# Optimization experiments

Measured on AMD Instinct MI355X. Metric: run time of the kernel, lower is better.

The kernel has to match this reference:

```python
import jax, jax.numpy as jnp
import numpy as np

EPS = 1e-18

_SOBEL_H = jnp.array([[-1., -2., -1.], [0., 0., 0.], [1., 2., 1.]], dtype=jnp.float32)


def _sobel_mag(x, eps):
    # x: [B,1,H,W]; depth-1 3x3 conv with 'same' padding, two fixed kernels
    wh = _SOBEL_H.reshape(1, 1, 3, 3).astype(x.dtype)   # horizontal kernel
    wv = _SOBEL_H.T.reshape(1, 1, 3, 3).astype(x.dtype)  # vertical kernel
    dn = jax.lax.conv_dimension_numbers(x.shape, wh.shape, ('NCHW', 'OIHW', 'NCHW'))
    gv = jax.lax.conv_general_dilated(x, wv, (1, 1), 'SAME', dimension_numbers=dn)
    gh = jax.lax.conv_general_dilated(x, wh, (1, 1), 'SAME', dimension_numbers=dn)
    return jnp.sqrt(gv * gv + gh * gh + eps)


def setup_inputs() -> dict:
    key = jax.random.key(0)
    k1, k2 = jax.random.split(key)
    shape = (64, 1, 512, 512)
    y_p = jax.random.uniform(k1, shape, dtype=jnp.float32)
    y_t = jax.random.uniform(k2, shape, dtype=jnp.float32)
    return {"y_p": y_p, "y_t": y_t}


def reference(y_p, y_t):
    eps = EPS
    ypg = _sobel_mag(y_p, eps)
    ytg = _sobel_mag(y_t, eps)
    out = (ytg - ypg) ** 2
    mask = (out == 0.0).astype(out.dtype)
    out = out + mask * eps
    out = jnp.sqrt(out + eps) * (1.0 - mask)
    return jnp.mean(out)
```

## Files before the change

kernel.cpp:

```cpp
#include <hip/hip_runtime.h>

#define IMG_W 512
#define IMG_H 512
#define BATCH 64
#define SLAB_ROWS 16
#define SLABS (IMG_H / SLAB_ROWS)
#define NBLOCKS (BATCH * SLABS)
#define NPIX (BATCH * IMG_W * IMG_H)

typedef float f32x4 __attribute__((ext_vector_type(4)));

__device__ __forceinline__ float fast_sqrtf(float x) {
    return __builtin_amdgcn_sqrtf(x);
}


#define GLOAD(dst, ptr)                                                        \
    asm volatile("global_load_dwordx4 %0, %1, off" : "=v"(dst) : "v"(ptr))

#define LOADR(I, A, B, IMG)                                                    \
    {                                                                          \
        int yy = ty - 1 + (I);                                                 \
        int yc = yy < 0 ? 0 : (yy > IMG_H - 1 ? IMG_H - 1 : yy);               \
        const float* r_ = (IMG) + ((size_t)yc << 9) + x0;                      \
        GLOAD(A, r_);                                                          \
        GLOAD(B, r_ + 4);                                                      \
    }

#define MKWIN(W, A, B)                                                         \
    float W[10];                                                               \
    {                                                                          \
        float l_ = __shfl_up((B)[3], 1, 64);                                   \
        float r_ = __shfl_down((A)[0], 1, 64);                                 \
        W[0] = (lane == 0) ? 0.f : l_;                                         \
        W[1] = (A)[0]; W[2] = (A)[1]; W[3] = (A)[2]; W[4] = (A)[3];            \
        W[5] = (B)[0]; W[6] = (B)[1]; W[7] = (B)[2]; W[8] = (B)[3];            \
        W[9] = (lane == 63) ? 0.f : r_;                                        \
    }

#define MKHS(HS, W)                                                            \
    float HS[8];                                                               \
    _Pragma("unroll")                                                          \
    for (int j = 0; j < 8; ++j)                                                \
        HS[j] = fmaf(2.f, W[j + 1], W[j]) + W[j + 2];

#define DO_OUT_P(O, WA, WB, WC, HSA, HSC)                                      \
    {                                                                          \
        float c_[10];                                                          \
        _Pragma("unroll")                                                      \
        for (int k = 0; k < 10; ++k)                                           \
            c_[k] = fmaf(2.f, WB[k], WA[k]) + WC[k];                           \
        _Pragma("unroll")                                                      \
        for (int j = 0; j < 8; ++j) {                                          \
            float gh = HSC[j] - HSA[j];                                        \
            float gv = c_[j + 2] - c_[j];                                      \
            magp[O][j] = fast_sqrtf(fmaf(gv, gv, fmaf(gh, gh, 1e-18f)));       \
        }                                                                      \
    }

#define DO_OUT_T(O, WA, WB, WC, HSA, HSC)                                      \
    {                                                                          \
        float c_[10];                                                          \
        _Pragma("unroll")                                                      \
        for (int k = 0; k < 10; ++k)                                           \
            c_[k] = fmaf(2.f, WB[k], WA[k]) + WC[k];                           \
        _Pragma("unroll")                                                      \
        for (int j = 0; j < 8; ++j) {                                          \
            float gh = HSC[j] - HSA[j];                                        \
            float gv = c_[j + 2] - c_[j];                                      \
            float mt = fast_sqrtf(fmaf(gv, gv, fmaf(gh, gh, 1e-18f)));         \
            lsum += fabsf(mt - magp[O][j]);     \
        }                                                                      \
    }

#define SOBEL_P(A0, B0, A1, B1, A2, B2, A3, B3, A4, B4, A5, B5)                \
    {                                                                          \
        MKWIN(w0_, A0, B0) MKWIN(w1_, A1, B1) MKWIN(w2_, A2, B2)               \
        MKWIN(w3_, A3, B3) MKWIN(w4_, A4, B4) MKWIN(w5_, A5, B5)               \
        MKHS(h0_, w0_) MKHS(h1_, w1_) MKHS(h2_, w2_)                           \
        MKHS(h3_, w3_) MKHS(h4_, w4_) MKHS(h5_, w5_)                           \
        DO_OUT_P(0, w0_, w1_, w2_, h0_, h2_)                                   \
        DO_OUT_P(1, w1_, w2_, w3_, h1_, h3_)                                   \
        DO_OUT_P(2, w2_, w3_, w4_, h2_, h4_)                                   \
        DO_OUT_P(3, w3_, w4_, w5_, h3_, h5_)                                   \
    }

#define SOBEL_T(A0, B0, A1, B1, A2, B2, A3, B3, A4, B4, A5, B5)                \
    {                                                                          \
        MKWIN(w0_, A0, B0) MKWIN(w1_, A1, B1) MKWIN(w2_, A2, B2)               \
        MKWIN(w3_, A3, B3) MKWIN(w4_, A4, B4) MKWIN(w5_, A5, B5)               \
        MKHS(h0_, w0_) MKHS(h1_, w1_) MKHS(h2_, w2_)                           \
        MKHS(h3_, w3_) MKHS(h4_, w4_) MKHS(h5_, w5_)                           \
        DO_OUT_T(0, w0_, w1_, w2_, h0_, h2_)                                   \
        DO_OUT_T(1, w1_, w2_, w3_, h1_, h3_)                                   \
        DO_OUT_T(2, w2_, w3_, w4_, h2_, h4_)                                   \
        DO_OUT_T(3, w3_, w4_, w5_, h3_, h5_)                                   \
    }

__global__ __launch_bounds__(256) void sobel_loss_kernel(
    const float* __restrict__ yp, const float* __restrict__ yt,
    float* __restrict__ bsums)
{
    __shared__ float wred[4];

    const int tid  = threadIdx.x;
    const int lane = tid & 63;
    const int bid  = blockIdx.x;
    const int b    = bid >> 5;
    const int slab = bid & (SLABS - 1);
    const int ty   = slab * SLAB_ROWS + ((tid >> 6) << 2);
    const int x0   = lane << 3;

    const float* imgp = yp + ((size_t)b << 18);
    const float* imgt = yt + ((size_t)b << 18);

    f32x4 A0p, B0p, A1p, B1p, A2p, B2p, A3p, B3p, A4p, B4p, A5p, B5p;
    f32x4 A0t, B0t, A1t, B1t, A2t, B2t, A3t, B3t, A4t, B4t, A5t, B5t;

    LOADR(0, A0p, B0p, imgp) LOADR(1, A1p, B1p, imgp) LOADR(2, A2p, B2p, imgp)
    LOADR(3, A3p, B3p, imgp) LOADR(4, A4p, B4p, imgp) LOADR(5, A5p, B5p, imgp)
    LOADR(0, A0t, B0t, imgt) LOADR(1, A1t, B1t, imgt) LOADR(2, A2t, B2t, imgt)
    LOADR(3, A3t, B3t, imgt) LOADR(4, A4t, B4t, imgt) LOADR(5, A5t, B5t, imgt)

    asm volatile("s_waitcnt vmcnt(12)"
                 : "+v"(A0p), "+v"(B0p), "+v"(A1p), "+v"(B1p),
                   "+v"(A2p), "+v"(B2p), "+v"(A3p), "+v"(B3p),
                   "+v"(A4p), "+v"(B4p), "+v"(A5p), "+v"(B5p));

    const f32x4 z4 = {0.f, 0.f, 0.f, 0.f};
    if (ty == 0)         { A0p = z4; B0p = z4; }
    if (ty + 4 == IMG_H) { A5p = z4; B5p = z4; }

    float magp[4][8];
    float lsum = 0.f;
    SOBEL_P(A0p, B0p, A1p, B1p, A2p, B2p, A3p, B3p, A4p, B4p, A5p, B5p)

    asm volatile("s_waitcnt vmcnt(0)"
                 : "+v"(A0t), "+v"(B0t), "+v"(A1t), "+v"(B1t),
                   "+v"(A2t), "+v"(B2t), "+v"(A3t), "+v"(B3t),
                   "+v"(A4t), "+v"(B4t), "+v"(A5t), "+v"(B5t));

    if (ty == 0)         { A0t = z4; B0t = z4; }
    if (ty + 4 == IMG_H) { A5t = z4; B5t = z4; }

    SOBEL_T(A0t, B0t, A1t, B1t, A2t, B2t, A3t, B3t, A4t, B4t, A5t, B5t)

#pragma unroll
    for (int off = 32; off > 0; off >>= 1)
        lsum += __shfl_down(lsum, off, 64);
    if (lane == 0) wred[tid >> 6] = lsum;
    __syncthreads();
    if (tid == 0)
        bsums[bid] = wred[0] + wred[1] + wred[2] + wred[3];
}

__global__ __launch_bounds__(256) void reduce_final(
    const float* __restrict__ bsums, float* __restrict__ out)
{
    __shared__ float wred[4];
    const int tid = threadIdx.x;
    float s = 0.f;
    for (int i = tid; i < NBLOCKS; i += 256) s += bsums[i];
#pragma unroll
    for (int off = 32; off > 0; off >>= 1)
        s += __shfl_down(s, off, 64);
    if ((tid & 63) == 0) wred[tid >> 6] = s;
    __syncthreads();
    if (tid == 0)
        out[0] = (wred[0] + wred[1] + wred[2] + wred[3]) * (1.0f / (float)NPIX);
}

extern "C" void kernel_launch(void* const* d_in, const int* in_sizes, int n_in,
                              void* d_out, int out_size, void* d_ws, size_t ws_size,
                              hipStream_t stream) {
    const float* yp = (const float*)d_in[0];
    const float* yt = (const float*)d_in[1];
    float* out = (float*)d_out;

    float* bsums = (float*)d_ws;
    sobel_loss_kernel<<<NBLOCKS, 256, 0, stream>>>(yp, yt, bsums);
    reduce_final<<<1, 256, 0, stream>>>(bsums, out);
}
```

Baseline: 144.4 us.

## Stage slab rows into LDS via global_load_lds and remap block order

Replaces the per-wave direct global loads of 6 overlapping rows with a cooperative stage of 18 rows per image into LDS using global_load_lds. Each wave then reads its rows from LDS, which removes the duplicated halo row fetches across waves. Blocks are also remapped with a stride-8 swizzle, likely to spread work across XCDs. In exchange the p and t loads are now serialized behind barriers, so the t load no longer overlaps the p compute, and the kernel uses about 36KB of LDS, which may cut occupancy.

After: 147.3 us. 2.0% more time.

```diff
diff --git a/kernel.cpp b/kernel.cpp
--- a/kernel.cpp
+++ b/kernel.cpp
@@ -7,6 +7,7 @@
 #define SLABS (IMG_H / SLAB_ROWS)
 #define NBLOCKS (BATCH * SLABS)
 #define NPIX (BATCH * IMG_W * IMG_H)
+#define LDS_ROWS 18
 
 typedef float f32x4 __attribute__((ext_vector_type(4)));
 
@@ -15,17 +16,12 @@
 }
 
 
-#define GLOAD(dst, ptr)                                                        \
-    asm volatile("global_load_dwordx4 %0, %1, off" : "=v"(dst) : "v"(ptr))
-
-#define LOADR(I, A, B, IMG)                                                    \
-    {                                                                          \
-        int yy = ty - 1 + (I);                                                 \
-        int yc = yy < 0 ? 0 : (yy > IMG_H - 1 ? IMG_H - 1 : yy);               \
-        const float* r_ = (IMG) + ((size_t)yc << 9) + x0;                      \
-        GLOAD(A, r_);                                                          \
-        GLOAD(B, r_ + 4);                                                      \
-    }
+typedef const __attribute__((address_space(1))) void gas_void;
+typedef __attribute__((address_space(3))) void las_void;
+
+__device__ __forceinline__ void gload_lds16(const float* g, float* l) {
+    __builtin_amdgcn_global_load_lds((gas_void*)g, (las_void*)l, 16, 0, 0);
+}
 
 #define MKWIN(W, A, B)                                                         \
     float W[10];                                                               \
@@ -97,61 +93,83 @@
         DO_OUT_T(3, w3_, w4_, w5_, h3_, h5_)                                   \
     }
 
+#define STAGE_IMG(IMG)                                                         \
+    {                                                                          \
+        _Pragma("unroll")                                                      \
+        for (int k = 0; k < 9; ++k) {                                          \
+            const int c = w * 9 + k;            \
+            int ys = row0 + (c >> 1);                                          \
+            ys = ys < 0 ? 0 : (ys > IMG_H - 1 ? IMG_H - 1 : ys);               \
+            gload_lds16((IMG) + ((size_t)ys << 9) + ((c & 1) << 8) + (lane << 2), \
+                        smem + (c << 8) + (lane << 2));                        \
+        }                                                                      \
+    }
+
+#define LDS_ROWS_TO_REGS()                                                     \
+    A0 = s4[rbase + 0 * 128 + cidx]; B0 = s4[rbase + 0 * 128 + cidx + 1];      \
+    A1 = s4[rbase + 1 * 128 + cidx]; B1 = s4[rbase + 1 * 128 + cidx + 1];      \
+    A2 = s4[rbase + 2 * 128 + cidx]; B2 = s4[rbase + 2 * 128 + cidx + 1];      \
+    A3 = s4[rbase + 3 * 128 + cidx]; B3 = s4[rbase + 3 * 128 + cidx + 1];      \
+    A4 = s4[rbase + 4 * 128 + cidx]; B4 = s4[rbase + 4 * 128 + cidx + 1];      \
+    A5 = s4[rbase + 5 * 128 + cidx]; B5 = s4[rbase + 5 * 128 + cidx + 1];
+
 __global__ __launch_bounds__(256) void sobel_loss_kernel(
     const float* __restrict__ yp, const float* __restrict__ yt,
     float* __restrict__ bsums)
 {
+    __shared__ float smem[LDS_ROWS * IMG_W];
     __shared__ float wred[4];
 
     const int tid  = threadIdx.x;
     const int lane = tid & 63;
-    const int bid  = blockIdx.x;
+    const int w    = tid >> 6;
+
+    const int bid0 = blockIdx.x;
+    const int bid  = (bid0 & 7) * (NBLOCKS / 8) + (bid0 >> 3);
+
     const int b    = bid >> 5;
     const int slab = bid & (SLABS - 1);
-    const int ty   = slab * SLAB_ROWS + ((tid >> 6) << 2);
-    const int x0   = lane << 3;
+    const int row0 = slab * SLAB_ROWS - 1;
+    const int ty   = slab * SLAB_ROWS + (w << 2);
 
     const float* imgp = yp + ((size_t)b << 18);
     const float* imgt = yt + ((size_t)b << 18);
 
-    f32x4 A0p, B0p, A1p, B1p, A2p, B2p, A3p, B3p, A4p, B4p, A5p, B5p;
-    f32x4 A0t, B0t, A1t, B1t, A2t, B2t, A3t, B3t, A4t, B4t, A5t, B5t;
-
-    LOADR(0, A0p, B0p, imgp) LOADR(1, A1p, B1p, imgp) LOADR(2, A2p, B2p, imgp)
-    LOADR(3, A3p, B3p, imgp) LOADR(4, A4p, B4p, imgp) LOADR(5, A5p, B5p, imgp)
-    LOADR(0, A0t, B0t, imgt) LOADR(1, A1t, B1t, imgt) LOADR(2, A2t, B2t, imgt)
-    LOADR(3, A3t, B3t, imgt) LOADR(4, A4t, B4t, imgt) LOADR(5, A5t, B5t, imgt)
-
-    asm volatile("s_waitcnt vmcnt(12)"
-                 : "+v"(A0p), "+v"(B0p), "+v"(A1p), "+v"(B1p),
-                   "+v"(A2p), "+v"(B2p), "+v"(A3p), "+v"(B3p),
-                   "+v"(A4p), "+v"(B4p), "+v"(A5p), "+v"(B5p));
+    const f32x4* s4 = (const f32x4*)smem;
+    const int rbase = (w << 2) * (IMG_W / 4);
+    const int cidx  = lane << 1;
 
     const f32x4 z4 = {0.f, 0.f, 0.f, 0.f};
-    if (ty == 0)         { A0p = z4; B0p = z4; }
-    if (ty + 4 == IMG_H) { A5p = z4; B5p = z4; }
+    f32x4 A0, B0, A1, B1, A2, B2, A3, B3, A4, B4, A5, B5;
 
     float magp[4][8];
     float lsum = 0.f;
-    SOBEL_P(A0p, B0p, A1p, B1p, A2p, B2p, A3p, B3p, A4p, B4p, A5p, B5p)
-
-    asm volatile("s_waitcnt vmcnt(0)"
-                 : "+v"(A0t), "+v"(B0t), "+v"(A1t), "+v"(B1t),
-                   "+v"(A2t), "+v"(B2t), "+v"(A3t), "+v"(B3t),
-                   "+v"(A4t), "+v"(B4t), "+v"(A5t), "+v"(B5t));
-
-    if (ty == 0)         { A0t = z4; B0t = z4; }
-    if (ty + 4 == IMG_H) { A5t = z4; B5t = z4; }
-
-    SOBEL_T(A0t, B0t, A1t, B1t, A2t, B2t, A3t, B3t, A4t, B4t, A5t, B5t)
+
+    STAGE_IMG(imgp)
+    __syncthreads();
+
+    LDS_ROWS_TO_REGS()
+    if (ty == 0)         { A0 = z4; B0 = z4; }
+    if (ty + 4 == IMG_H) { A5 = z4; B5 = z4; }
+    SOBEL_P(A0, B0, A1, B1, A2, B2, A3, B3, A4, B4, A5, B5)
+
+    __syncthreads();
+
+    STAGE_IMG(imgt)
+    __syncthreads();
+
+    LDS_ROWS_TO_REGS()
+    if (ty == 0)         { A0 = z4; B0 = z4; }
+    if (ty + 4 == IMG_H) { A5 = z4; B5 = z4; }
+    SOBEL_T(A0, B0, A1, B1, A2, B2, A3, B3, A4, B4, A5, B5)
 
 #pragma unroll
     for (int off = 32; off > 0; off >>= 1)
         lsum += __shfl_down(lsum, off, 64);
-    if (lane == 0) wred[tid >> 6] = lsum;
+    if (lane == 0) wred[w] = lsum;
     __syncthreads();
     if (tid == 0)
-        bsums[bid] = wred[0] + wred[1] + wred[2] + wred[3];
+        bsums[blockIdx.x] = wred[0] + wred[1] + wred[2] + wred[3];
 }
 
 __global__ __launch_bounds__(256) void reduce_final(
```

## Stage y_p slab into LDS via direct global-to-LDS loads, remap block order

Applied to the files above, without the earlier changes.

The predicted-image slab (18 rows including halo) is now loaded directly into shared memory with global_load_lds, so rows overlapping between the four wavefronts are fetched once instead of re-read from global memory. Each wave then reads its six rows from LDS into registers after a barrier. The target image keeps the old per-wave register loads. Block IDs are also permuted in a stride-8 pattern, likely to spread neighbouring slabs across XCDs/caches. This adds 36KB LDS per block, which may lower occupancy, and adds a barrier.

After: 148.3 us. 1.03x slower.

```diff
diff --git a/kernel.cpp b/kernel.cpp
--- a/kernel.cpp
+++ b/kernel.cpp
@@ -7,6 +7,7 @@
 #define SLABS (IMG_H / SLAB_ROWS)
 #define NBLOCKS (BATCH * SLABS)
 #define NPIX (BATCH * IMG_W * IMG_H)
+#define LDS_ROWS 18
 
 typedef float f32x4 __attribute__((ext_vector_type(4)));
 
@@ -14,6 +15,13 @@
     return __builtin_amdgcn_sqrtf(x);
 }
 
+
+typedef const __attribute__((address_space(1))) void gas_void;
+typedef __attribute__((address_space(3))) void las_void;
+
+__device__ __forceinline__ void gload_lds16(const float* g, float* l) {
+    __builtin_amdgcn_global_load_lds((gas_void*)g, (las_void*)l, 16, 0, 0);
+}
 
 #define GLOAD(dst, ptr)                                                        \
     asm volatile("global_load_dwordx4 %0, %1, off" : "=v"(dst) : "v"(ptr))
@@ -97,61 +105,88 @@
         DO_OUT_T(3, w3_, w4_, w5_, h3_, h5_)                                   \
     }
 
+#define STAGE_IMG(IMG)                                                         \
+    {                                                                          \
+        _Pragma("unroll")                                                      \
+        for (int k = 0; k < 9; ++k) {                                          \
+            const int c = w * 9 + k;            \
+            int ys = row0 + (c >> 1);                                          \
+            ys = ys < 0 ? 0 : (ys > IMG_H - 1 ? IMG_H - 1 : ys);               \
+            gload_lds16((IMG) + ((size_t)ys << 9) + ((c & 1) << 8) + (lane << 2), \
+                        smem + (c << 8) + (lane << 2));                        \
+        }                                                                      \
+    }
+
+#define LDS_ROWS_TO_REGS()                                                     \
+    A0p = s4[rbase + 0 * 128 + cidx]; B0p = s4[rbase + 0 * 128 + cidx + 1];    \
+    A1p = s4[rbase + 1 * 128 + cidx]; B1p = s4[rbase + 1 * 128 + cidx + 1];    \
+    A2p = s4[rbase + 2 * 128 + cidx]; B2p = s4[rbase + 2 * 128 + cidx + 1];    \
+    A3p = s4[rbase + 3 * 128 + cidx]; B3p = s4[rbase + 3 * 128 + cidx + 1];    \
+    A4p = s4[rbase + 4 * 128 + cidx]; B4p = s4[rbase + 4 * 128 + cidx + 1];    \
+    A5p = s4[rbase + 5 * 128 + cidx]; B5p = s4[rbase + 5 * 128 + cidx + 1];
+
 __global__ __launch_bounds__(256) void sobel_loss_kernel(
     const float* __restrict__ yp, const float* __restrict__ yt,
     float* __restrict__ bsums)
 {
+    __shared__ float smem[LDS_ROWS * IMG_W];
     __shared__ float wred[4];
 
     const int tid  = threadIdx.x;
     const int lane = tid & 63;
-    const int bid  = blockIdx.x;
+    const int w    = tid >> 6;
+
+    const int bid0 = blockIdx.x;
+    const int bid  = (bid0 & 7) * (NBLOCKS / 8) + (bid0 >> 3);
+
     const int b    = bid >> 5;
     const int slab = bid & (SLABS - 1);
-    const int ty   = slab * SLAB_ROWS + ((tid >> 6) << 2);
+    const int row0 = slab * SLAB_ROWS - 1;
+    const int ty   = slab * SLAB_ROWS + (w << 2);
     const int x0   = lane << 3;
 
     const float* imgp = yp + ((size_t)b << 18);
     const float* imgt = yt + ((size_t)b << 18);
 
+    const f32x4* s4 = (const f32x4*)smem;
+    const int rbase = (w << 2) * (IMG_W / 4);
+    const int cidx  = lane << 1;
+
+    const f32x4 z4 = {0.f, 0.f, 0.f, 0.f};
     f32x4 A0p, B0p, A1p, B1p, A2p, B2p, A3p, B3p, A4p, B4p, A5p, B5p;
     f32x4 A0t, B0t, A1t, B1t, A2t, B2t, A3t, B3t, A4t, B4t, A5t, B5t;
 
-    LOADR(0, A0p, B0p, imgp) LOADR(1, A1p, B1p, imgp) LOADR(2, A2p, B2p, imgp)
-    LOADR(3, A3p, B3p, imgp) LOADR(4, A4p, B4p, imgp) LOADR(5, A5p, B5p, imgp)
+    float magp[4][8];
+    float lsum = 0.f;
+
+    STAGE_IMG(imgp)
     LOADR(0, A0t, B0t, imgt) LOADR(1, A1t, B1t, imgt) LOADR(2, A2t, B2t, imgt)
     LOADR(3, A3t, B3t, imgt) LOADR(4, A4t, B4t, imgt) LOADR(5, A5t, B5t, imgt)
 
-    asm volatile("s_waitcnt vmcnt(12)"
-                 : "+v"(A0p), "+v"(B0p), "+v"(A1p), "+v"(B1p),
-                   "+v"(A2p), "+v"(B2p), "+v"(A3p), "+v"(B3p),
-                   "+v"(A4p), "+v"(B4p), "+v"(A5p), "+v"(B5p));
-
-    const f32x4 z4 = {0.f, 0.f, 0.f, 0.f};
+    asm volatile("s_waitcnt vmcnt(12)" ::: "memory");
+    __builtin_amdgcn_s_barrier();
+    __builtin_amdgcn_sched_barrier(0);
+
+    LDS_ROWS_TO_REGS()
     if (ty == 0)         { A0p = z4; B0p = z4; }
     if (ty + 4 == IMG_H) { A5p = z4; B5p = z4; }
-
-    float magp[4][8];
-    float lsum = 0.f;
     SOBEL_P(A0p, B0p, A1p, B1p, A2p, B2p, A3p, B3p, A4p, B4p, A5p, B5p)
 
     asm volatile("s_waitcnt vmcnt(0)"
                  : "+v"(A0t), "+v"(B0t), "+v"(A1t), "+v"(B1t),
                    "+v"(A2t), "+v"(B2t), "+v"(A3t), "+v"(B3t),
                    "+v"(A4t), "+v"(B4t), "+v"(A5t), "+v"(B5t));
-
     if (ty == 0)         { A0t = z4; B0t = z4; }
     if (ty + 4 == IMG_H) { A5t = z4; B5t = z4; }
-
     SOBEL_T(A0t, B0t, A1t, B1t, A2t, B2t, A3t, B3t, A4t, B4t, A5t, B5t)
 
 #pragma unroll
     for (int off = 32; off > 0; off >>= 1)
         lsum += __shfl_down(lsum, off, 64);
-    if (lane == 0) wred[tid >> 6] = lsum;
+    if (lane == 0) wred[w] = lsum;
     __syncthreads();
     if (tid == 0)
-        bsums[bid] = wred[0] + wred[1] + wred[2] + wred[3];
+        bsums[blockIdx.x] = wred[0] + wred[1] + wred[2] + wred[3];
 }
 
 __global__ __launch_bounds__(256) void reduce_final(
```

## Stream 16-row strips per wave with rolling row buffers and prefetch pipeline

Applied to the files above, without the earlier changes.

Each wave now processes a 16-row strip instead of a 4-row slab. It keeps a 6-deep ring of loaded rows and 3-deep horizontal-sum rings, issues loads three rows ahead, and overlaps them with compute through explicit vmcnt waits. This cuts halo re-reads from 6 loaded rows per 4 outputs to 18 per 16, and shrinks the grid to a quarter of the blocks. The risks are higher register pressure from the 2-wave launch bound and fewer blocks available to hide latency.

Result: no change. 144.9 us (+0.4%).

```diff
diff --git a/kernel.cpp b/kernel.cpp
--- a/kernel.cpp
+++ b/kernel.cpp
@@ -3,9 +3,10 @@
 #define IMG_W 512
 #define IMG_H 512
 #define BATCH 64
-#define SLAB_ROWS 16
-#define SLABS (IMG_H / SLAB_ROWS)
-#define NBLOCKS (BATCH * SLABS)
+#define STRIP_ROWS 16
+#define STRIPS_PER_IMG (IMG_H / STRIP_ROWS)
+#define NSTRIPS (BATCH * STRIPS_PER_IMG)
+#define NB_MAIN (NSTRIPS / 4)
 #define NPIX (BATCH * IMG_W * IMG_H)
 
 typedef float f32x4 __attribute__((ext_vector_type(4)));
@@ -18,86 +19,97 @@
 #define GLOAD(dst, ptr)                                                        \
     asm volatile("global_load_dwordx4 %0, %1, off" : "=v"(dst) : "v"(ptr))
 
-#define LOADR(I, A, B, IMG)                                                    \
+#define S6(k) (((k) + 1) % 6)
+#define S3(k) (((k) + 1) % 3)
+
+#define WEL(A, B, HL, HR, k, j)                                                \
+    ((j) == 0 ? HL[S3(k)]                                                      \
+              : ((j) == 9 ? HR[S3(k)]                                          \
+                          : ((j) <= 4 ? A[S6(k)][(j) - 1] : B[S6(k)][(j) - 5])))
+
+#define ISSUE(k, A, B, IMG)                                                    \
     {                                                                          \
-        int yy = ty - 1 + (I);                                                 \
-        int yc = yy < 0 ? 0 : (yy > IMG_H - 1 ? IMG_H - 1 : yy);               \
-        const float* r_ = (IMG) + ((size_t)yc << 9) + x0;                      \
-        GLOAD(A, r_);                                                          \
-        GLOAD(B, r_ + 4);                                                      \
+        int gy_ = stripy + (k);                                                \
+        gy_ = gy_ < 0 ? 0 : (gy_ > IMG_H - 1 ? IMG_H - 1 : gy_);               \
+        const float* r_ = (IMG) + ((size_t)gy_ << 9) + x0;                     \
+        GLOAD(A[S6(k)], r_);                                                   \
+        GLOAD(B[S6(k)], r_ + 4);                                               \
     }
 
-#define MKWIN(W, A, B)                                                         \
-    float W[10];                                                               \
+#define PREP(k, A, B, HL, HR, HS)                                              \
     {                                                                          \
-        float l_ = __shfl_up((B)[3], 1, 64);                                   \
-        float r_ = __shfl_down((A)[0], 1, 64);                                 \
-        W[0] = (lane == 0) ? 0.f : l_;                                         \
-        W[1] = (A)[0]; W[2] = (A)[1]; W[3] = (A)[2]; W[4] = (A)[3];            \
-        W[5] = (B)[0]; W[6] = (B)[1]; W[7] = (B)[2]; W[8] = (B)[3];            \
-        W[9] = (lane == 63) ? 0.f : r_;                                        \
+        float l_ = __shfl_up(B[S6(k)][3], 1, 64);                              \
+        float r_ = __shfl_down(A[S6(k)][0], 1, 64);                            \
+        HL[S3(k)] = (lane == 0) ? 0.f : l_;                                    \
+        HR[S3(k)] = (lane == 63) ? 0.f : r_;                                   \
+        _Pragma("unroll")                                                      \
+        for (int j = 0; j < 8; ++j)                                            \
+            HS[S3(k)][j] = fmaf(2.f, WEL(A, B, HL, HR, k, j + 1),              \
+                                WEL(A, B, HL, HR, k, j)) +                     \
+                           WEL(A, B, HL, HR, k, j + 2);                        \
     }
 
-#define MKHS(HS, W)                                                            \
-    float HS[8];                                                               \
-    _Pragma("unroll")                                                          \
-    for (int j = 0; j < 8; ++j)                                                \
-        HS[j] = fmaf(2.f, W[j + 1], W[j]) + W[j + 2];
-
-#define DO_OUT_P(O, WA, WB, WC, HSA, HSC)                                      \
+#define OUT_P(r)                                                               \
     {                                                                          \
-        float c_[10];                                                          \
+        float c9_[10];                                                         \
         _Pragma("unroll")                                                      \
-        for (int k = 0; k < 10; ++k)                                           \
-            c_[k] = fmaf(2.f, WB[k], WA[k]) + WC[k];                           \
+        for (int j = 0; j < 10; ++j)                                           \
+            c9_[j] = fmaf(2.f, WEL(pA, pB, hlP, hrP, (r), j),                  \
+                          WEL(pA, pB, hlP, hrP, (r)-1, j)) +                   \
+                     WEL(pA, pB, hlP, hrP, (r) + 1, j);                        \
         _Pragma("unroll")                                                      \
         for (int j = 0; j < 8; ++j) {                                          \
-            float gh = HSC[j] - HSA[j];                                        \
-            float gv = c_[j + 2] - c_[j];                                      \
-            magp[O][j] = fast_sqrtf(fmaf(gv, gv, fmaf(gh, gh, 1e-18f)));       \
+            float gh = hsP[S3((r) + 1)][j] - hsP[S3((r)-1)][j];                \
+            float gv = c9_[j + 2] - c9_[j];                                    \
+            magrow[j] = fast_sqrtf(fmaf(gv, gv, fmaf(gh, gh, 1e-18f)));        \
         }                                                                      \
     }
 
-#define DO_OUT_T(O, WA, WB, WC, HSA, HSC)                                      \
+#define OUT_T(r)                                                               \
     {                                                                          \
-        float c_[10];                                                          \
+        float c9_[10];                                                         \
         _Pragma("unroll")                                                      \
-        for (int k = 0; k < 10; ++k)                                           \
-            c_[k] = fmaf(2.f, WB[k], WA[k]) + WC[k];                           \
+        for (int j = 0; j < 10; ++j)                                           \
+            c9_[j] = fmaf(2.f, WEL(tA, tB, hlT, hrT, (r), j),                  \
+                          WEL(tA, tB, hlT, hrT, (r)-1, j)) +                   \
+                     WEL(tA, tB, hlT, hrT, (r) + 1, j);                        \
         _Pragma("unroll")                                                      \
         for (int j = 0; j < 8; ++j) {                                          \
-            float gh = HSC[j] - HSA[j];                                        \
-            float gv = c_[j + 2] - c_[j];                                      \
+            float gh = hsT[S3((r) + 1)][j] - hsT[S3((r)-1)][j];                \
+            float gv = c9_[j + 2] - c9_[j];                                    \
             float mt = fast_sqrtf(fmaf(gv, gv, fmaf(gh, gh, 1e-18f)));         \
-            lsum += fabsf(mt - magp[O][j]);     \
+            lsum += fabsf(mt - magrow[j]);      \
         }                                                                      \
     }
 
-#define SOBEL_P(A0, B0, A1, B1, A2, B2, A3, B3, A4, B4, A5, B5)                \
+#define ITER(r, WP, WT)                                                        \
     {                                                                          \
-        MKWIN(w0_, A0, B0) MKWIN(w1_, A1, B1) MKWIN(w2_, A2, B2)               \
-        MKWIN(w3_, A3, B3) MKWIN(w4_, A4, B4) MKWIN(w5_, A5, B5)               \
-        MKHS(h0_, w0_) MKHS(h1_, w1_) MKHS(h2_, w2_)                           \
-        MKHS(h3_, w3_) MKHS(h4_, w4_) MKHS(h5_, w5_)                           \
-        DO_OUT_P(0, w0_, w1_, w2_, h0_, h2_)                                   \
-        DO_OUT_P(1, w1_, w2_, w3_, h1_, h3_)                                   \
-        DO_OUT_P(2, w2_, w3_, w4_, h2_, h4_)                                   \
-        DO_OUT_P(3, w3_, w4_, w5_, h3_, h5_)                                   \
+        float magrow[8];                                                       \
+        asm volatile("s_waitcnt vmcnt(" #WP ")" ::: "memory");                 \
+        __builtin_amdgcn_sched_barrier(0);                                     \
+        if ((r) == 0 && stop_) { pA[S6(-1)] = z4; pB[S6(-1)] = z4; }           \
+        if ((r) == 15 && sbot_) { pA[S6(16)] = z4; pB[S6(16)] = z4; }          \
+        if ((r) == 0) {                                                        \
+            PREP(-1, pA, pB, hlP, hrP, hsP)                                    \
+            PREP(0, pA, pB, hlP, hrP, hsP)                                     \
+        }                                                                      \
+        PREP((r) + 1, pA, pB, hlP, hrP, hsP)                                   \
+        if ((r) <= 13) ISSUE((r) + 3, pA, pB, imgp)                            \
+        OUT_P(r)                                                               \
+        asm volatile("s_waitcnt vmcnt(" #WT ")" ::: "memory");                 \
+        __builtin_amdgcn_sched_barrier(0);                                     \
+        if ((r) == 0 && stop_) { tA[S6(-1)] = z4; tB[S6(-1)] = z4; }           \
+        if ((r) == 15 && sbot_) { tA[S6(16)] = z4; tB[S6(16)] = z4; }          \
+        if ((r) == 0) {                                                        \
+            PREP(-1, tA, tB, hlT, hrT, hsT)                                    \
+            PREP(0, tA, tB, hlT, hrT, hsT)                                     \
+        }                                                                      \
+        PREP((r) + 1, tA, tB, hlT, hrT, hsT)                                   \
+        if ((r) <= 13) ISSUE((r) + 3, tA, tB, imgt)                            \
+        OUT_T(r)                                                               \
     }
 
-#define SOBEL_T(A0, B0, A1, B1, A2, B2, A3, B3, A4, B4, A5, B5)                \
-    {                                                                          \
-        MKWIN(w0_, A0, B0) MKWIN(w1_, A1, B1) MKWIN(w2_, A2, B2)               \
-        MKWIN(w3_, A3, B3) MKWIN(w4_, A4, B4) MKWIN(w5_, A5, B5)               \
-        MKHS(h0_, w0_) MKHS(h1_, w1_) MKHS(h2_, w2_)                           \
-        MKHS(h3_, w3_) MKHS(h4_, w4_) MKHS(h5_, w5_)                           \
-        DO_OUT_T(0, w0_, w1_, w2_, h0_, h2_)                                   \
-        DO_OUT_T(1, w1_, w2_, w3_, h1_, h3_)                                   \
-        DO_OUT_T(2, w2_, w3_, w4_, h2_, h4_)                                   \
-        DO_OUT_T(3, w3_, w4_, w5_, h3_, h5_)                                   \
-    }
-
-__global__ __launch_bounds__(256) void sobel_loss_kernel(
+__global__ __launch_bounds__(256, 2) void sobel_loss_kernel(
     const float* __restrict__ yp, const float* __restrict__ yt,
     float* __restrict__ bsums)
 {
@@ -105,50 +117,41 @@
 
     const int tid  = threadIdx.x;
     const int lane = tid & 63;
-    const int bid  = blockIdx.x;
-    const int b    = bid >> 5;
-    const int slab = bid & (SLABS - 1);
-    const int ty   = slab * SLAB_ROWS + ((tid >> 6) << 2);
-    const int x0   = lane << 3;
+    const int w    = tid >> 6;
+
+    const int bid   = blockIdx.x;
+    const int b     = bid >> 3;
+    const int strip = ((bid & 7) << 2) + w;
+    const int stripy = strip << 4;
+    const int x0    = lane << 3;
+
+    const bool stop_ = (strip == 0);
+    const bool sbot_ = (strip == STRIPS_PER_IMG - 1);
 
     const float* imgp = yp + ((size_t)b << 18);
     const float* imgt = yt + ((size_t)b << 18);
 
-    f32x4 A0p, B0p, A1p, B1p, A2p, B2p, A3p, B3p, A4p, B4p, A5p, B5p;
-    f32x4 A0t, B0t, A1t, B1t, A2t, B2t, A3t, B3t, A4t, B4t, A5t, B5t;
-
-    LOADR(0, A0p, B0p, imgp) LOADR(1, A1p, B1p, imgp) LOADR(2, A2p, B2p, imgp)
-    LOADR(3, A3p, B3p, imgp) LOADR(4, A4p, B4p, imgp) LOADR(5, A5p, B5p, imgp)
-    LOADR(0, A0t, B0t, imgt) LOADR(1, A1t, B1t, imgt) LOADR(2, A2t, B2t, imgt)
-    LOADR(3, A3t, B3t, imgt) LOADR(4, A4t, B4t, imgt) LOADR(5, A5t, B5t, imgt)
-
-    asm volatile("s_waitcnt vmcnt(12)"
-                 : "+v"(A0p), "+v"(B0p), "+v"(A1p), "+v"(B1p),
-                   "+v"(A2p), "+v"(B2p), "+v"(A3p), "+v"(B3p),
-                   "+v"(A4p), "+v"(B4p), "+v"(A5p), "+v"(B5p));
+    f32x4 pA[6], pB[6], tA[6], tB[6];
+    float hlP[3], hrP[3], hlT[3], hrT[3];
+    float hsP[3][8], hsT[3][8];
 
     const f32x4 z4 = {0.f, 0.f, 0.f, 0.f};
-    if (ty == 0)         { A0p = z4; B0p = z4; }
-    if (ty + 4 == IMG_H) { A5p = z4; B5p = z4; }
+    float lsum = 0.f;
 
-    float magp[4][8];
-    float lsum = 0.f;
-    SOBEL_P(A0p, B0p, A1p, B1p, A2p, B2p, A3p, B3p, A4p, B4p, A5p, B5p)
+    ISSUE(-1, pA, pB, imgp) ISSUE(-1, tA, tB, imgt)
+    ISSUE(0,  pA, pB, imgp) ISSUE(0,  tA, tB, imgt)
+    ISSUE(1,  pA, pB, imgp) ISSUE(1,  tA, tB, imgt)
+    ISSUE(2,  pA, pB, imgp) ISSUE(2,  tA, tB, imgt)
 
-    asm volatile("s_waitcnt vmcnt(0)"
-                 : "+v"(A0t), "+v"(B0t), "+v"(A1t), "+v"(B1t),
-                   "+v"(A2t), "+v"(B2t), "+v"(A3t), "+v"(B3t),
-                   "+v"(A4t), "+v"(B4t), "+v"(A5t), "+v"(B5t));
-
-    if (ty == 0)         { A0t = z4; B0t = z4; }
-    if (ty + 4 == IMG_H) { A5t = z4; B5t = z4; }
-
-    SOBEL_T(A0t, B0t, A1t, B1t, A2t, B2t, A3t, B3t, A4t, B4t, A5t, B5t)
+    ITER(0, 6, 6)  ITER(1, 6, 6)  ITER(2, 6, 6)  ITER(3, 6, 6)
+    ITER(4, 6, 6)  ITER(5, 6, 6)  ITER(6, 6, 6)  ITER(7, 6, 6)
+    ITER(8, 6, 6)  ITER(9, 6, 6)  ITER(10, 6, 6) ITER(11, 6, 6)
+    ITER(12, 6, 6) ITER(13, 6, 6) ITER(14, 6, 4) ITER(15, 2, 0)
 
 #pragma unroll
     for (int off = 32; off > 0; off >>= 1)
         lsum += __shfl_down(lsum, off, 64);
-    if (lane == 0) wred[tid >> 6] = lsum;
+    if (lane == 0) wred[w] = lsum;
     __syncthreads();
     if (tid == 0)
         bsums[bid] = wred[0] + wred[1] + wred[2] + wred[3];
@@ -160,7 +163,7 @@
     __shared__ float wred[4];
     const int tid = threadIdx.x;
     float s = 0.f;
-    for (int i = tid; i < NBLOCKS; i += 256) s += bsums[i];
+    for (int i = tid; i < NB_MAIN; i += 256) s += bsums[i];
 #pragma unroll
     for (int off = 32; off > 0; off >>= 1)
         s += __shfl_down(s, off, 64);
@@ -178,6 +181,6 @@
     float* out = (float*)d_out;
 
     float* bsums = (float*)d_ws;
-    sobel_loss_kernel<<<NBLOCKS, 256, 0, stream>>>(yp, yt, bsums);
+    sobel_loss_kernel<<<NB_MAIN, 256, 0, stream>>>(yp, yt, bsums);
     reduce_final<<<1, 256, 0, stream>>>(bsums, out);
 }
```
